# Performance work log

Measured on AMD Instinct MI355X. Metric: run time of the kernel, lower is better.

## Reference

```python
import jax, jax.numpy as jnp
import numpy as np

PERIODS = [4, 2, 1]   # base_periods[:n_period]
TEMPERATURE = 0.1
TOPM = 20
EPS = 1e-12


def _l2norm(v, axis):
    n = jnp.sqrt(jnp.sum(v * v, axis=axis, keepdims=True))
    return v / jnp.maximum(n, EPS)


def decompose_mg(x):
    """x: [B, L, C] -> mg: [G, B, L, C] (offset removed, as in torch code)."""
    B, L, C = x.shape
    mg = []
    for g in PERIODS:
        cur = x.reshape(B, L // g, g, C).mean(axis=2)      # unfold(size=g, step=g).mean(-1)
        cur = jnp.repeat(cur, g, axis=1)                   # repeat_interleave back to L
        mg.append(cur)
    mg = jnp.stack(mg, axis=0)                             # [G, B, L, C]
    return mg - mg[:, :, -1:, :]                           # remove per-series last-step offset


def extract_channel_state(mg):
    """mg: [G, B, L, C] -> [G, B, C, 4] (mean, std, slope, mean |diff|)."""
    L = mg.shape[2]
    mean = mg.mean(axis=2)
    std = mg.std(axis=2)                                   # unbiased=False (ddof=0)
    slope = (mg[:, :, -1, :] - mg[:, :, 0, :]) / float(L - 1)
    abs_diff = jnp.abs(mg[:, :, 1:, :] - mg[:, :, :-1, :]).mean(axis=2)
    return jnp.stack([mean, std, slope, abs_diff], axis=-1)


def setup_inputs() -> dict:
    key = jax.random.key(0)
    k1, k2, k3 = jax.random.split(key, 3)
    B, L, C, G, T, P = 32, 512, 64, 3, 10000, 96
    x = jax.random.normal(k1, (B, L, C), dtype=jnp.float32)
    pool_state = jax.random.normal(k2, (G, T, C, 4), dtype=jnp.float32)
    y_pool = jax.random.normal(k3, (T, P, C), dtype=jnp.float32)
    return {"x": x, "pool_state": pool_state, "y_pool": y_pool}


def reference(x, pool_state, y_pool):
    # Multi-scale decomposition of query batch
    q_mg = decompose_mg(x)                                  # [G, B, L, C]
    q_state = extract_channel_state(q_mg)                   # [G, B, C, 4]
    # Normalized channel-state similarity vs candidate pool
    q = _l2norm(q_state, axis=-1)
    p = _l2norm(pool_state, axis=-1)
    sim = jnp.einsum('gbcd,gtcd->gbct', q, p)               # [G, B, C, T]
    sim = sim.mean(axis=0)                                  # combine granularities -> [B, C, T]
    # Top-m retrieval per (batch, channel)
    vals, idx = jax.lax.top_k(sim, TOPM)                    # [B, C, M]
    w = jax.nn.softmax(vals / TEMPERATURE, axis=-1)         # [B, C, M]
    # Gather retrieved future windows, channelwise: y_pool [T, P, C]
    C = y_pool.shape[2]
    y_ct = jnp.transpose(y_pool, (2, 0, 1))                 # [C, T, P]
    gathered = y_ct[jnp.arange(C)[None, :, None], idx]      # [B, C, M, P]
    out = jnp.einsum('bcm,bcmp->bpc', w, gathered)          # [B, P, C]
    return out
```

## Files before the change

kernel.cpp:

```cpp
#include <hip/hip_runtime.h>
#include <math.h>

#define NB 32
#define NL 512
#define NC 64
#define NG 3
#define NT 10000
#define NP 96
#define TOPM 20
#define M1 8
#define NCH 256
#define CHUNK 40
#define QK 16
#define NCAND 64
#define GSTR ((size_t)NT * NC * 4)

__global__ __launch_bounds__(512) void pre_kernel(const float* __restrict__ x,
                                                  const float* __restrict__ ps,
                                                  double* __restrict__ q,
                                                  float* __restrict__ phat) {
  __shared__ double s_sum[8][3][64], s_sq[8][3][64], s_abs[8][3][64];
  __shared__ double s_first[3][64], s_last[3][64];
  if (blockIdx.x < NB) {
    const int b = blockIdx.x, w = threadIdx.x >> 6, c = threadIdx.x & 63;
    const float* xp = x + (size_t)b * NL * NC + c;
    const int l0 = w * 64;
    double sum[3] = {0, 0, 0}, sumsq[3] = {0, 0, 0}, sumabs[3] = {0, 0, 0};
    double prev[3] = {0, 0, 0}, first[3] = {0, 0, 0};
    if (w > 0) {
      double e0 = xp[(l0 - 4) * NC], e1 = xp[(l0 - 3) * NC];
      double e2 = xp[(l0 - 2) * NC], e3 = xp[(l0 - 1) * NC];
      prev[2] = e3; prev[1] = (e2 + e3) * 0.5; prev[0] = (e0 + e1 + e2 + e3) * 0.25;
    }
    double acc2 = 0.0, acc4 = 0.0;
    for (int i = 0; i < 64; ++i) {
      const int l = l0 + i;
      double v = (double)xp[l * NC];
      sum[2] += v; sumsq[2] += v * v;
      if (l == 0) first[2] = v; else sumabs[2] += fabs(v - prev[2]);
      prev[2] = v;
      acc2 += v;
      if (l & 1) {
        double cur = acc2 * 0.5; acc2 = 0.0;
        sum[1] += cur; sumsq[1] += cur * cur;
        if (l == 1) first[1] = cur; else sumabs[1] += fabs(cur - prev[1]);
        prev[1] = cur;
      }
      acc4 += v;
      if ((l & 3) == 3) {
        double cur = acc4 * 0.25; acc4 = 0.0;
        sum[0] += cur; sumsq[0] += cur * cur;
        if (l == 3) first[0] = cur; else sumabs[0] += fabs(cur - prev[0]);
        prev[0] = cur;
      }
    }
    for (int g = 0; g < 3; ++g) {
      s_sum[w][g][c] = sum[g]; s_sq[w][g][c] = sumsq[g]; s_abs[w][g][c] = sumabs[g];
    }
    if (w == 0) { for (int g = 0; g < 3; ++g) s_first[g][c] = first[g]; }
    if (w == 7) { for (int g = 0; g < 3; ++g) s_last[g][c] = prev[g]; }
    __syncthreads();
    if (w == 0) {
      const double J[3] = {128.0, 256.0, 512.0};
      for (int g = 0; g < 3; ++g) {
        double S = 0, Q2 = 0, A = 0;
        for (int ww = 0; ww < 8; ++ww) {
          S += s_sum[ww][g][c]; Q2 += s_sq[ww][g][c]; A += s_abs[ww][g][c];
        }
        double mean = S / J[g];
        double var = Q2 / J[g] - mean * mean; if (var < 0.0) var = 0.0;
        double last = s_last[g][c];
        double s0 = mean - last;
        double s1 = sqrt(var);
        double s2 = (last - s_first[g][c]) * (1.0 / 511.0);
        double s3 = A * (1.0 / 511.0);
        double n = sqrt(s0 * s0 + s1 * s1 + s2 * s2 + s3 * s3);
        double inv = 1.0 / fmax(n, 1e-12);
        double* qp = q + ((((size_t)g * NB) + b) * NC + c) * 4;
        qp[0] = s0 * inv; qp[1] = s1 * inv; qp[2] = s2 * inv; qp[3] = s3 * inv;
      }
    }
  } else {
    const int i = (blockIdx.x - NB) * 512 + threadIdx.x;
    if (i < NT * NC) {
      const int t = i >> 6, c = i & 63;
#pragma unroll
      for (int g = 0; g < 3; ++g) {
        const size_t off = ((((size_t)g * NT) + t) * NC + c) * 4;
        const float4 pv = *reinterpret_cast<const float4*>(ps + off);
        double p0 = pv.x, p1 = pv.y, p2 = pv.z, p3 = pv.w;
        double inv = 1.0 / fmax(sqrt(p0 * p0 + p1 * p1 + p2 * p2 + p3 * p3), 1e-12);
        float4 o;
        o.x = (float)(p0 * inv); o.y = (float)(p1 * inv);
        o.z = (float)(p2 * inv); o.w = (float)(p3 * inv);
        *reinterpret_cast<float4*>(phat + off) = o;
      }
    }
  }
}

__device__ __forceinline__ void insert8(float s, int ti, float val[M1], int idx[M1]) {
  float cv = s; int ci = ti;
#pragma unroll
  for (int m = 0; m < M1; ++m) {
    bool sw = cv > val[m];
    float tv = sw ? val[m] : cv; int tx = sw ? idx[m] : ci;
    val[m] = sw ? cv : val[m];   idx[m] = sw ? ci : idx[m];
    cv = tv; ci = tx;
  }
}

__global__ __launch_bounds__(1024, 8) void sim32_kernel(
    const float* __restrict__ phat, const double* __restrict__ q,
    float* __restrict__ cval, int* __restrict__ cidx) {
  const int wav = threadIdx.x >> 6;
  const int c = threadIdx.x & 63;
  const int b = blockIdx.x * 16 + wav;
  const int ch = blockIdx.y;
  float qv[12];
#pragma unroll
  for (int g = 0; g < 3; ++g) {
    const double* qp = q + ((((size_t)g * NB) + b) * NC + c) * 4;
#pragma unroll
    for (int j = 0; j < 4; ++j) qv[g * 4 + j] = (float)(qp[j] * (1.0 / 3.0));
  }
  float val[M1]; int idx[M1];
#pragma unroll
  for (int m = 0; m < M1; ++m) { val[m] = -1e30f; idx[m] = 0; }
  int t0 = ch * CHUNK;
  int t1 = t0 + CHUNK; if (t1 > NT) t1 = NT;
  for (int t = t0; t + 1 < t1; t += 2) {
    const size_t oA = ((size_t)t * NC + c) * 4;
    const size_t oB = ((size_t)(t + 1) * NC + c) * 4;
    const float4 a0 = *reinterpret_cast<const float4*>(phat + oA);
    const float4 a1 = *reinterpret_cast<const float4*>(phat + GSTR + oA);
    const float4 a2 = *reinterpret_cast<const float4*>(phat + 2 * GSTR + oA);
    const float4 b0 = *reinterpret_cast<const float4*>(phat + oB);
    const float4 b1 = *reinterpret_cast<const float4*>(phat + GSTR + oB);
    const float4 b2 = *reinterpret_cast<const float4*>(phat + 2 * GSTR + oB);
    float sA = qv[0] * a0.x + qv[1] * a0.y + qv[2] * a0.z + qv[3] * a0.w +
               qv[4] * a1.x + qv[5] * a1.y + qv[6] * a1.z + qv[7] * a1.w +
               qv[8] * a2.x + qv[9] * a2.y + qv[10] * a2.z + qv[11] * a2.w;
    float sB = qv[0] * b0.x + qv[1] * b0.y + qv[2] * b0.z + qv[3] * b0.w +
               qv[4] * b1.x + qv[5] * b1.y + qv[6] * b1.z + qv[7] * b1.w +
               qv[8] * b2.x + qv[9] * b2.y + qv[10] * b2.z + qv[11] * b2.w;
    if (sA > val[M1 - 1]) insert8(sA, t, val, idx);
    if (sB > val[M1 - 1]) insert8(sB, t + 1, val, idx);
  }
  float* vo = cval + ((((size_t)b * NC) + c) * NCH + ch) * M1;
  int* io = cidx + ((((size_t)b * NC) + c) * NCH + ch) * M1;
#pragma unroll
  for (int m = 0; m < M1; ++m) { vo[m] = val[m]; io[m] = idx[m]; }
}

__device__ __forceinline__ unsigned long long mk_key(float v, int t) {
  unsigned u = __float_as_uint(v);
  u = (u & 0x80000000u) ? ~u : (u | 0x80000000u);
  return ((unsigned long long)u << 32) | (unsigned long long)(0xFFFFFFFFu - (unsigned)t);
}

__global__ __launch_bounds__(128) void merge_gather_kernel(
    const float* __restrict__ cval, const int* __restrict__ cidx,
    const float* __restrict__ ps, const double* __restrict__ q,
    const float* __restrict__ y, float* __restrict__ out) {
  const int c = blockIdx.x, b = blockIdx.y;
  __shared__ float v_s[NCH * M1];
  __shared__ int i_s[NCH * M1];
  __shared__ int ct_s[NCAND];
  __shared__ double rv_s[NCAND];
  __shared__ double m0_s, inv_s;
  __shared__ double e_s[TOPM];
  __shared__ float w_s[TOPM];
  __shared__ int ts_s[TOPM];
  const int n = NCH * M1;
  const size_t row = (size_t)b * NC + c;
  const float4* vin = reinterpret_cast<const float4*>(cval + row * n);
  const int4* iin = reinterpret_cast<const int4*>(cidx + row * n);
  for (int k = threadIdx.x; k < n / 4; k += 128) {
    *reinterpret_cast<float4*>(&v_s[k * 4]) = vin[k];
    *reinterpret_cast<int4*>(&i_s[k * 4]) = iin[k];
  }
  __syncthreads();
  {
    const int w = threadIdx.x >> 6, lane = threadIdx.x & 63;
    const int lane32 = lane & 31;
    const int qtr = (w << 1) | (lane >> 5);
    const int l0 = (qtr * 64 + lane32 * 2) * M1;
    const int l1 = l0 + M1;
    int p0 = 0, p1 = 0;
    unsigned long long k0 = mk_key(v_s[l0], i_s[l0]);
    unsigned long long k1 = mk_key(v_s[l1], i_s[l1]);
    for (int r = 0; r < QK; ++r) {
      unsigned long long me = k0 > k1 ? k0 : k1;
      unsigned long long km = me;
#pragma unroll
      for (int st = 1; st < 32; st <<= 1) {
        unsigned long long k2 = __shfl_xor(km, st);
        km = k2 > km ? k2 : km;
      }
      if (lane32 == r)
        ct_s[qtr * QK + r] = (int)(0xFFFFFFFFu - (unsigned)(km & 0xFFFFFFFFull));
      if (me == km) {
        if (k0 >= k1) {
          ++p0;
          k0 = (p0 < M1) ? mk_key(v_s[l0 + p0], i_s[l0 + p0]) : 0ull;
        } else {
          ++p1;
          k1 = (p1 < M1) ? mk_key(v_s[l1 + p1], i_s[l1 + p1]) : 0ull;
        }
      }
    }
  }
  __syncthreads();
  if (threadIdx.x < NCAND) {
    const int t = ct_s[threadIdx.x];
    double s = 0.0;
#pragma unroll
    for (int g = 0; g < 3; ++g) {
      const double* qp = q + ((((size_t)g * NB) + b) * NC + c) * 4;
      const float4 pv = *reinterpret_cast<const float4*>(
          ps + ((((size_t)g * NT) + t) * NC + c) * 4);
      double pp0 = pv.x, pp1 = pv.y, pp2 = pv.z, pp3 = pv.w;
      double ss = pp0 * pp0 + pp1 * pp1 + pp2 * pp2 + pp3 * pp3;
      double dot = qp[0] * pp0 + qp[1] * pp1 + qp[2] * pp2 + qp[3] * pp3;
      s += dot / fmax(sqrt(ss), 1e-12);
    }
    rv_s[threadIdx.x] = s * (1.0 / 3.0);
  }
  __syncthreads();
  if (threadIdx.x < NCAND) {
    const double v = rv_s[threadIdx.x];
    const int t = ct_s[threadIdx.x];
    int rank = 0;
    for (int j = 0; j < NCAND; ++j) {
      double vj = rv_s[j]; int tj = ct_s[j];
      rank += (vj > v) || (vj == v && tj < t);
    }
    if (rank == 0) m0_s = v;
    __syncthreads();
    if (rank < TOPM) {
      e_s[rank] = exp((v - m0_s) * 10.0);
      ts_s[rank] = t;
    }
    __syncthreads();
    if (threadIdx.x == 0) {
      double sum = 0.0;
#pragma unroll
      for (int m = 0; m < TOPM; ++m) sum += e_s[m];
      inv_s = 1.0 / sum;
    }
    __syncthreads();
    if (threadIdx.x < TOPM) w_s[threadIdx.x] = (float)(e_s[threadIdx.x] * inv_s);
  } else {
    __syncthreads(); __syncthreads(); __syncthreads();
  }
  __syncthreads();
  const int p = threadIdx.x;
  if (p < NP) {
    float acc = 0.f;
#pragma unroll
    for (int m = 0; m < TOPM; ++m)
      acc += w_s[m] * y[(((size_t)ts_s[m]) * NP + p) * NC + c];
    out[(((size_t)b * NP) + p) * NC + c] = acc;
  }
}

__global__ __launch_bounds__(256) void sim_topk_inline_kernel(
    const float* __restrict__ ps, const double* __restrict__ q,
    double* __restrict__ cval, int* __restrict__ cidx, int nch, int chunk) {
  const int wav = threadIdx.x >> 6;
  const int c = threadIdx.x & 63;
  const int b = blockIdx.y * 4 + wav;
  const int ch = blockIdx.x;
  double qv[3][4];
#pragma unroll
  for (int g = 0; g < 3; ++g) {
    const double* qp = q + ((((size_t)g * NB) + b) * NC + c) * 4;
    qv[g][0] = qp[0]; qv[g][1] = qp[1]; qv[g][2] = qp[2]; qv[g][3] = qp[3];
  }
  double val[TOPM]; int idx[TOPM];
#pragma unroll
  for (int m = 0; m < TOPM; ++m) { val[m] = -1e300; idx[m] = 0; }
  int t0 = ch * chunk;
  int t1 = t0 + chunk; if (t1 > NT) t1 = NT;
  for (int t = t0; t < t1; ++t) {
    double s = 0.0;
#pragma unroll
    for (int g = 0; g < 3; ++g) {
      const float4 pv = *reinterpret_cast<const float4*>(
          ps + ((((size_t)g * NT) + t) * NC + c) * 4);
      double p0 = pv.x, p1 = pv.y, p2 = pv.z, p3 = pv.w;
      double ss = p0 * p0 + p1 * p1 + p2 * p2 + p3 * p3;
      double dot = qv[g][0] * p0 + qv[g][1] * p1 + qv[g][2] * p2 + qv[g][3] * p3;
      s += dot / fmax(sqrt(ss), 1e-12);
    }
    s *= (1.0 / 3.0);
    if (s > val[TOPM - 1]) {
// ... 40 lines not shown
          cv = tv; ci = ti;
        }
      }
    }
    double mx = val[0];
    double e[TOPM]; double sum = 0.0;
#pragma unroll
    for (int m = 0; m < TOPM; ++m) { e[m] = exp((val[m] - mx) * 10.0); sum += e[m]; }
    double inv = 1.0 / sum;
#pragma unroll
    for (int m = 0; m < TOPM; ++m) { w_s[m] = (float)(e[m] * inv); i_s[m] = idx[m]; }
  }
  __syncthreads();
  const int p = threadIdx.x;
  if (p < NP) {
    float acc = 0.f;
#pragma unroll
    for (int m = 0; m < TOPM; ++m)
      acc += w_s[m] * y[(((size_t)i_s[m]) * NP + p) * NC + c];
    out[(((size_t)b * NP) + p) * NC + c] = acc;
  }
}

extern "C" void kernel_launch(void* const* d_in, const int* in_sizes, int n_in,
                              void* d_out, int out_size, void* d_ws, size_t ws_size,
                              hipStream_t stream) {
  const float* x = (const float*)d_in[0];
  const float* ps = (const float*)d_in[1];
  const float* y = (const float*)d_in[2];
  float* out = (float*)d_out;
  char* ws = (char*)d_ws;

  const size_t qbytes = (size_t)NG * NB * NC * 4 * sizeof(double);
  const size_t phat32bytes = (size_t)NG * NT * NC * 4 * sizeof(float);
  const size_t cvalbytes = (size_t)NB * NC * NCH * M1 * sizeof(float);
  const size_t cidxbytes = (size_t)NB * NC * NCH * M1 * sizeof(int);

  double* qbuf = (double*)ws;

  if (ws_size >= qbytes + phat32bytes + cvalbytes + cidxbytes) {
    float* phat = (float*)(ws + qbytes);
    float* cval = (float*)(ws + qbytes + phat32bytes);
    int* cidx = (int*)((char*)cval + cvalbytes);
    const int pn_blocks = (NT * NC + 511) / 512;
    pre_kernel<<<dim3(NB + pn_blocks), dim3(512), 0, stream>>>(x, ps, qbuf, phat);
    sim32_kernel<<<dim3(NB / 16, NCH), dim3(1024), 0, stream>>>(phat, qbuf, cval, cidx);
    merge_gather_kernel<<<dim3(NC, NB), dim3(128), 0, stream>>>(cval, cidx, ps, qbuf,
                                                                y, out);
  } else {
    pre_kernel<<<dim3(NB), dim3(512), 0, stream>>>(x, ps, qbuf, (float*)nullptr);
    const size_t per_ch = (size_t)NB * NC * TOPM * (sizeof(double) + sizeof(int));
    int nch = 1;
    if (ws_size > qbytes) {
      size_t mc = (ws_size - qbytes) / per_ch;
      nch = mc < 32 ? (int)mc : 32;
      if (nch < 1) nch = 1;
    }
    const int chunk = (NT + nch - 1) / nch;
    double* cval = (double*)(ws + qbytes);
    int* cidx = (int*)((char*)cval + (size_t)NB * NC * nch * TOPM * sizeof(double));
    sim_topk_inline_kernel<<<dim3(nch, NB / 4), dim3(256), 0, stream>>>(
        ps, qbuf, cval, cidx, nch, chunk);
    merge_gather_old_kernel<<<dim3(NC, NB), dim3(128), 0, stream>>>(cval, cidx, y, out, nch);
  }
}
```

Measured before the change: 139.1 us.

## Fuse pool normalization into similarity kernel and pack candidates into one buffer

Removes the separate pass that normalized pool_state into a float workspace copy. The similarity kernel now reads raw pool_state and applies rsqrt-based normalization inline, which avoids writing and re-reading a ~30MB buffer but adds per-element normalization math. Candidate values and indices are packed into one interleaved 64-byte record per chunk and written with vector stores. The merge/gather kernel grows to 256 threads and splits the 20-way gather across two halves, with indices sorted for locality. Launch bounds on the sim kernel drop from occupancy 8 to 4.

```diff
diff --git a/kernel.cpp b/kernel.cpp
--- a/kernel.cpp
+++ b/kernel.cpp
@@ -15,86 +15,66 @@
 #define NCAND 64
 #define GSTR ((size_t)NT * NC * 4)
 
-__global__ __launch_bounds__(512) void pre_kernel(const float* __restrict__ x,
-                                                  const float* __restrict__ ps,
-                                                  double* __restrict__ q,
-                                                  float* __restrict__ phat) {
+__global__ __launch_bounds__(512) void qstat_kernel(const float* __restrict__ x,
+                                                    double* __restrict__ q) {
   __shared__ double s_sum[8][3][64], s_sq[8][3][64], s_abs[8][3][64];
   __shared__ double s_first[3][64], s_last[3][64];
-  if (blockIdx.x < NB) {
-    const int b = blockIdx.x, w = threadIdx.x >> 6, c = threadIdx.x & 63;
-    const float* xp = x + (size_t)b * NL * NC + c;
-    const int l0 = w * 64;
-    double sum[3] = {0, 0, 0}, sumsq[3] = {0, 0, 0}, sumabs[3] = {0, 0, 0};
-    double prev[3] = {0, 0, 0}, first[3] = {0, 0, 0};
-    if (w > 0) {
-      double e0 = xp[(l0 - 4) * NC], e1 = xp[(l0 - 3) * NC];
-      double e2 = xp[(l0 - 2) * NC], e3 = xp[(l0 - 1) * NC];
-      prev[2] = e3; prev[1] = (e2 + e3) * 0.5; prev[0] = (e0 + e1 + e2 + e3) * 0.25;
-    }
-    double acc2 = 0.0, acc4 = 0.0;
-    for (int i = 0; i < 64; ++i) {
-      const int l = l0 + i;
-      double v = (double)xp[l * NC];
-      sum[2] += v; sumsq[2] += v * v;
-      if (l == 0) first[2] = v; else sumabs[2] += fabs(v - prev[2]);
-      prev[2] = v;
-      acc2 += v;
-      if (l & 1) {
-        double cur = acc2 * 0.5; acc2 = 0.0;
-        sum[1] += cur; sumsq[1] += cur * cur;
-        if (l == 1) first[1] = cur; else sumabs[1] += fabs(cur - prev[1]);
-        prev[1] = cur;
+  const int b = blockIdx.x, w = threadIdx.x >> 6, c = threadIdx.x & 63;
+  const float* xp = x + (size_t)b * NL * NC + c;
+  const int l0 = w * 64;
+  double sum[3] = {0, 0, 0}, sumsq[3] = {0, 0, 0}, sumabs[3] = {0, 0, 0};
+  double prev[3] = {0, 0, 0}, first[3] = {0, 0, 0};
+  if (w > 0) {
+    double e0 = xp[(l0 - 4) * NC], e1 = xp[(l0 - 3) * NC];
+    double e2 = xp[(l0 - 2) * NC], e3 = xp[(l0 - 1) * NC];
+    prev[2] = e3; prev[1] = (e2 + e3) * 0.5; prev[0] = (e0 + e1 + e2 + e3) * 0.25;
+  }
+  double acc2 = 0.0, acc4 = 0.0;
+  for (int i = 0; i < 64; ++i) {
+    const int l = l0 + i;
+    double v = (double)xp[l * NC];
+    sum[2] += v; sumsq[2] += v * v;
+    if (l == 0) first[2] = v; else sumabs[2] += fabs(v - prev[2]);
+    prev[2] = v;
+    acc2 += v;
+    if (l & 1) {
+      double cur = acc2 * 0.5; acc2 = 0.0;
+      sum[1] += cur; sumsq[1] += cur * cur;
+      if (l == 1) first[1] = cur; else sumabs[1] += fabs(cur - prev[1]);
+      prev[1] = cur;
+    }
+    acc4 += v;
+    if ((l & 3) == 3) {
+      double cur = acc4 * 0.25; acc4 = 0.0;
+      sum[0] += cur; sumsq[0] += cur * cur;
+      if (l == 3) first[0] = cur; else sumabs[0] += fabs(cur - prev[0]);
+      prev[0] = cur;
+    }
+  }
+  for (int g = 0; g < 3; ++g) {
+    s_sum[w][g][c] = sum[g]; s_sq[w][g][c] = sumsq[g]; s_abs[w][g][c] = sumabs[g];
+  }
+  if (w == 0) { for (int g = 0; g < 3; ++g) s_first[g][c] = first[g]; }
+  if (w == 7) { for (int g = 0; g < 3; ++g) s_last[g][c] = prev[g]; }
+  __syncthreads();
+  if (w == 0) {
+    const double J[3] = {128.0, 256.0, 512.0};
+    for (int g = 0; g < 3; ++g) {
+      double S = 0, Q2 = 0, A = 0;
+      for (int ww = 0; ww < 8; ++ww) {
+        S += s_sum[ww][g][c]; Q2 += s_sq[ww][g][c]; A += s_abs[ww][g][c];
       }
-      acc4 += v;
-      if ((l & 3) == 3) {
-        double cur = acc4 * 0.25; acc4 = 0.0;
-        sum[0] += cur; sumsq[0] += cur * cur;
-        if (l == 3) first[0] = cur; else sumabs[0] += fabs(cur - prev[0]);
-        prev[0] = cur;
-      }
-    }
-    for (int g = 0; g < 3; ++g) {
-      s_sum[w][g][c] = sum[g]; s_sq[w][g][c] = sumsq[g]; s_abs[w][g][c] = sumabs[g];
-    }
-    if (w == 0) { for (int g = 0; g < 3; ++g) s_first[g][c] = first[g]; }
-    if (w == 7) { for (int g = 0; g < 3; ++g) s_last[g][c] = prev[g]; }
-    __syncthreads();
-    if (w == 0) {
-      const double J[3] = {128.0, 256.0, 512.0};
-      for (int g = 0; g < 3; ++g) {
-        double S = 0, Q2 = 0, A = 0;
-        for (int ww = 0; ww < 8; ++ww) {
-          S += s_sum[ww][g][c]; Q2 += s_sq[ww][g][c]; A += s_abs[ww][g][c];
-        }
-        double mean = S / J[g];
-        double var = Q2 / J[g] - mean * mean; if (var < 0.0) var = 0.0;
-        double last = s_last[g][c];
-        double s0 = mean - last;
-        double s1 = sqrt(var);
-        double s2 = (last - s_first[g][c]) * (1.0 / 511.0);
-        double s3 = A * (1.0 / 511.0);
-        double n = sqrt(s0 * s0 + s1 * s1 + s2 * s2 + s3 * s3);
-        double inv = 1.0 / fmax(n, 1e-12);
-        double* qp = q + ((((size_t)g * NB) + b) * NC + c) * 4;
-        qp[0] = s0 * inv; qp[1] = s1 * inv; qp[2] = s2 * inv; qp[3] = s3 * inv;
-      }
-    }
-  } else {
-    const int i = (blockIdx.x - NB) * 512 + threadIdx.x;
-    if (i < NT * NC) {
-      const int t = i >> 6, c = i & 63;
-#pragma unroll
-      for (int g = 0; g < 3; ++g) {
-        const size_t off = ((((size_t)g * NT) + t) * NC + c) * 4;
-        const float4 pv = *reinterpret_cast<const float4*>(ps + off);
-        double p0 = pv.x, p1 = pv.y, p2 = pv.z, p3 = pv.w;
-        double inv = 1.0 / fmax(sqrt(p0 * p0 + p1 * p1 + p2 * p2 + p3 * p3), 1e-12);
-        float4 o;
-        o.x = (float)(p0 * inv); o.y = (float)(p1 * inv);
-        o.z = (float)(p2 * inv); o.w = (float)(p3 * inv);
-        *reinterpret_cast<float4*>(phat + off) = o;
-      }
+      double mean = S / J[g];
+      double var = Q2 / J[g] - mean * mean; if (var < 0.0) var = 0.0;
+      double last = s_last[g][c];
+      double s0 = mean - last;
+      double s1 = sqrt(var);
+      double s2 = (last - s_first[g][c]) * (1.0 / 511.0);
+      double s3 = A * (1.0 / 511.0);
+      double n = sqrt(s0 * s0 + s1 * s1 + s2 * s2 + s3 * s3);
+      double inv = 1.0 / fmax(n, 1e-12);
+      double* qp = q + ((((size_t)g * NB) + b) * NC + c) * 4;
+      qp[0] = s0 * inv; qp[1] = s1 * inv; qp[2] = s2 * inv; qp[3] = s3 * inv;
     }
   }
 }
@@ -110,9 +90,17 @@
   }
 }
 
-__global__ __launch_bounds__(1024, 8) void sim32_kernel(
-    const float* __restrict__ phat, const double* __restrict__ q,
-    float* __restrict__ cval, int* __restrict__ cidx) {
+__device__ __forceinline__ float dot4(float4 a, float q0, float q1, float q2, float q3) {
+  return q0 * a.x + q1 * a.y + q2 * a.z + q3 * a.w;
+}
+__device__ __forceinline__ float nrm4(float4 a) {
+  float ss = a.x * a.x + a.y * a.y + a.z * a.z + a.w * a.w;
+  return rsqrtf(ss < 1e-24f ? 1e-24f : ss);
+}
+
+__global__ __launch_bounds__(1024, 4) void sim32_kernel(
+    const float* __restrict__ ps, const double* __restrict__ q,
+    float* __restrict__ cand) {
   const int wav = threadIdx.x >> 6;
   const int c = threadIdx.x & 63;
   const int b = blockIdx.x * 16 + wav;
@@ -131,26 +119,31 @@
   int t1 = t0 + CHUNK; if (t1 > NT) t1 = NT;
   for (int t = t0; t + 1 < t1; t += 2) {
     const size_t oA = ((size_t)t * NC + c) * 4;
-    const size_t oB = ((size_t)(t + 1) * NC + c) * 4;
-    const float4 a0 = *reinterpret_cast<const float4*>(phat + oA);
-    const float4 a1 = *reinterpret_cast<const float4*>(phat + GSTR + oA);
-    const float4 a2 = *reinterpret_cast<const float4*>(phat + 2 * GSTR + oA);
-    const float4 b0 = *reinterpret_cast<const float4*>(phat + oB);
-    const float4 b1 = *reinterpret_cast<const float4*>(phat + GSTR + oB);
-    const float4 b2 = *reinterpret_cast<const float4*>(phat + 2 * GSTR + oB);
-    float sA = qv[0] * a0.x + qv[1] * a0.y + qv[2] * a0.z + qv[3] * a0.w +
-               qv[4] * a1.x + qv[5] * a1.y + qv[6] * a1.z + qv[7] * a1.w +
-               qv[8] * a2.x + qv[9] * a2.y + qv[10] * a2.z + qv[11] * a2.w;
-    float sB = qv[0] * b0.x + qv[1] * b0.y + qv[2] * b0.z + qv[3] * b0.w +
-               qv[4] * b1.x + qv[5] * b1.y + qv[6] * b1.z + qv[7] * b1.w +
-               qv[8] * b2.x + qv[9] * b2.y + qv[10] * b2.z + qv[11] * b2.w;
+    const size_t oB = oA + (size_t)NC * 4;
+    const float4 a0 = *reinterpret_cast<const float4*>(ps + oA);
+    const float4 a1 = *reinterpret_cast<const float4*>(ps + GSTR + oA);
+    const float4 a2 = *reinterpret_cast<const float4*>(ps + 2 * GSTR + oA);
+    const float4 b0 = *reinterpret_cast<const float4*>(ps + oB);
+    const float4 b1 = *reinterpret_cast<const float4*>(ps + GSTR + oB);
+    const float4 b2 = *reinterpret_cast<const float4*>(ps + 2 * GSTR + oB);
+    float sA = dot4(a0, qv[0], qv[1], qv[2], qv[3]) * nrm4(a0) +
+               dot4(a1, qv[4], qv[5], qv[6], qv[7]) * nrm4(a1) +
+               dot4(a2, qv[8], qv[9], qv[10], qv[11]) * nrm4(a2);
+    float sB = dot4(b0, qv[0], qv[1], qv[2], qv[3]) * nrm4(b0) +
+               dot4(b1, qv[4], qv[5], qv[6], qv[7]) * nrm4(b1) +
+               dot4(b2, qv[8], qv[9], qv[10], qv[11]) * nrm4(b2);
     if (sA > val[M1 - 1]) insert8(sA, t, val, idx);
     if (sB > val[M1 - 1]) insert8(sB, t + 1, val, idx);
   }
-  float* vo = cval + ((((size_t)b * NC) + c) * NCH + ch) * M1;
-  int* io = cidx + ((((size_t)b * NC) + c) * NCH + ch) * M1;
-#pragma unroll
-  for (int m = 0; m < M1; ++m) { vo[m] = val[m]; io[m] = idx[m]; }
+  float* bp = cand + ((((size_t)b * NC) + c) * NCH + ch) * 16;
+  float4 f0 = make_float4(val[0], val[1], val[2], val[3]);
+  float4 f1 = make_float4(val[4], val[5], val[6], val[7]);
+  int4 j0 = make_int4(idx[0], idx[1], idx[2], idx[3]);
+  int4 j1 = make_int4(idx[4], idx[5], idx[6], idx[7]);
+  reinterpret_cast<float4*>(bp)[0] = f0;
+  reinterpret_cast<float4*>(bp)[1] = f1;
+  reinterpret_cast<int4*>(bp)[2] = j0;
+  reinterpret_cast<int4*>(bp)[3] = j1;
 }
 
 __device__ __forceinline__ unsigned long long mk_key(float v, int t) {
@@ -159,10 +152,10 @@
   return ((unsigned long long)u << 32) | (unsigned long long)(0xFFFFFFFFu - (unsigned)t);
 }
 
-__global__ __launch_bounds__(128) void merge_gather_kernel(
-    const float* __restrict__ cval, const int* __restrict__ cidx,
-    const float* __restrict__ ps, const double* __restrict__ q,
-    const float* __restrict__ y, float* __restrict__ out) {
+__global__ __launch_bounds__(256) void merge_gather_kernel(
+    const float* __restrict__ cand, const float* __restrict__ ps,
+    const double* __restrict__ q, const float* __restrict__ y,
+    float* __restrict__ out) {
   const int c = blockIdx.x, b = blockIdx.y;
   __shared__ float v_s[NCH * M1];
   __shared__ int i_s[NCH * M1];
@@ -170,18 +163,26 @@
   __shared__ double rv_s[NCAND];
   __shared__ double m0_s, inv_s;
   __shared__ double e_s[TOPM];
-  __shared__ float w_s[TOPM];
   __shared__ int ts_s[TOPM];
-  const int n = NCH * M1;
+  __shared__ float w2_s[TOPM];
+  __shared__ int t2_s[TOPM];
+  __shared__ float part_s[2][NP];
   const size_t row = (size_t)b * NC + c;
-  const float4* vin = reinterpret_cast<const float4*>(cval + row * n);
-  const int4* iin = reinterpret_cast<const int4*>(cidx + row * n);
-  for (int k = threadIdx.x; k < n / 4; k += 128) {
-    *reinterpret_cast<float4*>(&v_s[k * 4]) = vin[k];
-    *reinterpret_cast<int4*>(&i_s[k * 4]) = iin[k];
-  }
-  __syncthreads();
-  {
+  const float4* blob = reinterpret_cast<const float4*>(cand + row * NCH * 16);
+  for (int k = threadIdx.x; k < NCH * 4; k += 256) {
+    float4 f = blob[k];
+    const int ch = k >> 2, part = k & 3;
+    if (part < 2) {
+      const int o = ch * M1 + part * 4;
+      v_s[o] = f.x; v_s[o + 1] = f.y; v_s[o + 2] = f.z; v_s[o + 3] = f.w;
+    } else {
+      const int o = ch * M1 + (part - 2) * 4;
+      int4 j = *reinterpret_cast<int4*>(&f);
+      i_s[o] = j.x; i_s[o + 1] = j.y; i_s[o + 2] = j.z; i_s[o + 3] = j.w;
+    }
+  }
+  __syncthreads();
+  if (threadIdx.x < 128) {
     const int w = threadIdx.x >> 6, lane = threadIdx.x & 63;
     const int lane32 = lane & 31;
     const int qtr = (w << 1) | (lane >> 5);
@@ -202,67 +203,76 @@
         ct_s[qtr * QK + r] = (int)(0xFFFFFFFFu - (unsigned)(km & 0xFFFFFFFFull));
       if (me == km) {
         if (k0 >= k1) {
-          ++p0;
-          k0 = (p0 < M1) ? mk_key(v_s[l0 + p0], i_s[l0 + p0]) : 0ull;
+          ++p0; k0 = (p0 < M1) ? mk_key(v_s[l0 + p0], i_s[l0 + p0]) : 0ull;
         } else {
-          ++p1;
-          k1 = (p1 < M1) ? mk_key(v_s[l1 + p1], i_s[l1 + p1]) : 0ull;
+          ++p1; k1 = (p1 < M1) ? mk_key(v_s[l1 + p1], i_s[l1 + p1]) : 0ull;
         }
       }
     }
   }
   __syncthreads();
+  double myv = -1e300; int myt = 0x7fffffff;
   if (threadIdx.x < NCAND) {
-    const int t = ct_s[threadIdx.x];
+    myt = ct_s[threadIdx.x];
     double s = 0.0;
 #pragma unroll
     for (int g = 0; g < 3; ++g) {
       const double* qp = q + ((((size_t)g * NB) + b) * NC + c) * 4;
       const float4 pv = *reinterpret_cast<const float4*>(
-          ps + ((((size_t)g * NT) + t) * NC + c) * 4);
+          ps + ((((size_t)g * NT) + myt) * NC + c) * 4);
       double pp0 = pv.x, pp1 = pv.y, pp2 = pv.z, pp3 = pv.w;
       double ss = pp0 * pp0 + pp1 * pp1 + pp2 * pp2 + pp3 * pp3;
       double dot = qp[0] * pp0 + qp[1] * pp1 + qp[2] * pp2 + qp[3] * pp3;
       s += dot / fmax(sqrt(ss), 1e-12);
     }
-    rv_s[threadIdx.x] = s * (1.0 / 3.0);
-  }
-  __syncthreads();
+    myv = s * (1.0 / 3.0);
+    rv_s[threadIdx.x] = myv;
+  }
+  __syncthreads();
+  int rank = -1;
   if (threadIdx.x < NCAND) {
-    const double v = rv_s[threadIdx.x];
-    const int t = ct_s[threadIdx.x];
-    int rank = 0;
+    rank = 0;
     for (int j = 0; j < NCAND; ++j) {
       double vj = rv_s[j]; int tj = ct_s[j];
-      rank += (vj > v) || (vj == v && tj < t);
-    }
-    if (rank == 0) m0_s = v;
-    __syncthreads();
-    if (rank < TOPM) {
-      e_s[rank] = exp((v - m0_s) * 10.0);
-      ts_s[rank] = t;
-    }
-    __syncthreads();
-    if (threadIdx.x == 0) {
-      double sum = 0.0;
-#pragma unroll
-      for (int m = 0; m < TOPM; ++m) sum += e_s[m];
-      inv_s = 1.0 / sum;
-    }
-    __syncthreads();
-    if (threadIdx.x < TOPM) w_s[threadIdx.x] = (float)(e_s[threadIdx.x] * inv_s);
-  } else {
-    __syncthreads(); __syncthreads(); __syncthreads();
-  }
-  __syncthreads();
-  const int p = threadIdx.x;
-  if (p < NP) {
+      rank += (vj > myv) || (vj == myv && tj < myt);
+    }
+    if (rank == 0) m0_s = myv;
+  }
+  __syncthreads();
+  if (rank >= 0 && rank < TOPM) { e_s[rank] = exp((myv - m0_s) * 10.0); ts_s[rank] = myt; }
+  __syncthreads();
+  if (threadIdx.x == 0) {
+    double sum = 0.0;
+#pragma unroll
+    for (int m = 0; m < TOPM; ++m) sum += e_s[m];
+    inv_s = 1.0 / sum;
+  }
+  __syncthreads();
+  if (threadIdx.x < TOPM) {
+    const int t = ts_s[threadIdx.x];
+    int pos = 0;
+#pragma unroll
+    for (int j = 0; j < TOPM; ++j) pos += (ts_s[j] < t);
+    w2_s[pos] = (float)(e_s[threadIdx.x] * inv_s);
+    t2_s[pos] = t;
+  }
+  __syncthreads();
+  const int half = threadIdx.x >> 7;
+  const int pp = threadIdx.x & 127;
+  if (pp < NP) {
     float acc = 0.f;
-#pragma unroll
-    for (int m = 0; m < TOPM; ++m)
-      acc += w_s[m] * y[(((size_t)ts_s[m]) * NP + p) * NC + c];
-    out[(((size_t)b * NP) + p) * NC + c] = acc;
-  }
+    const float* yc = y + c;
+#pragma unroll
+    for (int m = 0; m < 10; ++m) {
+      const int mm = half * 10 + m;
+      acc += w2_s[mm] * yc[((size_t)t2_s[mm] * NP + pp) << 6];
+    }
+    part_s[half][pp] = acc;
+  }
+  __syncthreads();
+  if (threadIdx.x < NP)
+    out[(((size_t)b * NP) + threadIdx.x) * NC + c] =
+        part_s[0][threadIdx.x] + part_s[1][threadIdx.x];
 }
 
 __global__ __launch_bounds__(256) void sim_topk_inline_kernel(
@@ -369,23 +379,17 @@
   char* ws = (char*)d_ws;
 
   const size_t qbytes = (size_t)NG * NB * NC * 4 * sizeof(double);
-  const size_t phat32bytes = (size_t)NG * NT * NC * 4 * sizeof(float);
-  const size_t cvalbytes = (size_t)NB * NC * NCH * M1 * sizeof(float);
-  const size_t cidxbytes = (size_t)NB * NC * NCH * M1 * sizeof(int);
+  const size_t candbytes = (size_t)NB * NC * NCH * 16 * sizeof(float);
 
   double* qbuf = (double*)ws;
 
-  if (ws_size >= qbytes + phat32bytes + cvalbytes + cidxbytes) {
-    float* phat = (float*)(ws + qbytes);
-    float* cval = (float*)(ws + qbytes + phat32bytes);
-    int* cidx = (int*)((char*)cval + cvalbytes);
-    const int pn_blocks = (NT * NC + 511) / 512;
-    pre_kernel<<<dim3(NB + pn_blocks), dim3(512), 0, stream>>>(x, ps, qbuf, phat);
-    sim32_kernel<<<dim3(NB / 16, NCH), dim3(1024), 0, stream>>>(phat, qbuf, cval, cidx);
-    merge_gather_kernel<<<dim3(NC, NB), dim3(128), 0, stream>>>(cval, cidx, ps, qbuf,
-                                                                y, out);
+  if (ws_size >= qbytes + candbytes) {
+    float* cand = (float*)(ws + qbytes);
+    qstat_kernel<<<dim3(NB), dim3(512), 0, stream>>>(x, qbuf);
+    sim32_kernel<<<dim3(NB / 16, NCH), dim3(1024), 0, stream>>>(ps, qbuf, cand);
+    merge_gather_kernel<<<dim3(NC, NB), dim3(256), 0, stream>>>(cand, ps, qbuf, y, out);
   } else {
-    pre_kernel<<<dim3(NB), dim3(512), 0, stream>>>(x, ps, qbuf, (float*)nullptr);
+    qstat_kernel<<<dim3(NB), dim3(512), 0, stream>>>(x, qbuf);
     const size_t per_ch = (size_t)NB * NC * TOPM * (sizeof(double) + sizeof(int));
     int nch = 1;
     if (ws_size > qbytes) {
```

Result: slower. 156.2 us (+12.3%).

## Pre-transpose y_pool to channel-major fp16 for contiguous gather reads

Applied to the files above, without the earlier changes.

Adds a block range to the prep kernel that transposes the 236 MB y_pool into a [C,T,P] half-precision buffer via LDS, so the final gather reads contiguous P-runs per channel instead of strided 4-byte loads. The transpose runs every call and must read all of y_pool and write a 123 MB buffer, which is far more traffic than the sparse gather (B*C*20*96 elements) it replaces. Output precision also drops to fp16 for the retrieved windows. The merge kernel's synchronization structure is also flattened.

```diff
diff --git a/kernel.cpp b/kernel.cpp
--- a/kernel.cpp
+++ b/kernel.cpp
@@ -1,4 +1,5 @@
 #include <hip/hip_runtime.h>
+#include <hip/hip_fp16.h>
 #include <math.h>
 
 #define NB 32
@@ -13,15 +14,21 @@
 #define CHUNK 40
 #define QK 16
 #define NCAND 64
+#define PNBLK 1250
+#define TRBLK 5000
 #define GSTR ((size_t)NT * NC * 4)
 
-__global__ __launch_bounds__(512) void pre_kernel(const float* __restrict__ x,
-                                                  const float* __restrict__ ps,
-                                                  double* __restrict__ q,
-                                                  float* __restrict__ phat) {
-  __shared__ double s_sum[8][3][64], s_sq[8][3][64], s_abs[8][3][64];
-  __shared__ double s_first[3][64], s_last[3][64];
+__global__ __launch_bounds__(512) void prep_kernel(
+    const float* __restrict__ x, const float* __restrict__ ps,
+    const float* __restrict__ y, double* __restrict__ q,
+    float* __restrict__ phat, __half* __restrict__ yt16) {
+  __shared__ __align__(16) char smem[50176];
   if (blockIdx.x < NB) {
+    double* s_sum = (double*)smem;
+    double* s_sq = s_sum + 1536;
+    double* s_abs = s_sq + 1536;
+    double* s_first = s_abs + 1536;
+    double* s_last = s_first + 192;
     const int b = blockIdx.x, w = threadIdx.x >> 6, c = threadIdx.x & 63;
     const float* xp = x + (size_t)b * NL * NC + c;
     const int l0 = w * 64;
@@ -55,24 +62,28 @@
       }
     }
     for (int g = 0; g < 3; ++g) {
-      s_sum[w][g][c] = sum[g]; s_sq[w][g][c] = sumsq[g]; s_abs[w][g][c] = sumabs[g];
-    }
-    if (w == 0) { for (int g = 0; g < 3; ++g) s_first[g][c] = first[g]; }
-    if (w == 7) { for (int g = 0; g < 3; ++g) s_last[g][c] = prev[g]; }
+      s_sum[w * 192 + g * 64 + c] = sum[g];
+      s_sq[w * 192 + g * 64 + c] = sumsq[g];
+      s_abs[w * 192 + g * 64 + c] = sumabs[g];
+    }
+    if (w == 0) { for (int g = 0; g < 3; ++g) s_first[g * 64 + c] = first[g]; }
+    if (w == 7) { for (int g = 0; g < 3; ++g) s_last[g * 64 + c] = prev[g]; }
     __syncthreads();
     if (w == 0) {
       const double J[3] = {128.0, 256.0, 512.0};
       for (int g = 0; g < 3; ++g) {
         double S = 0, Q2 = 0, A = 0;
         for (int ww = 0; ww < 8; ++ww) {
-          S += s_sum[ww][g][c]; Q2 += s_sq[ww][g][c]; A += s_abs[ww][g][c];
+          S += s_sum[ww * 192 + g * 64 + c];
+          Q2 += s_sq[ww * 192 + g * 64 + c];
+          A += s_abs[ww * 192 + g * 64 + c];
         }
         double mean = S / J[g];
         double var = Q2 / J[g] - mean * mean; if (var < 0.0) var = 0.0;
-        double last = s_last[g][c];
+        double last = s_last[g * 64 + c];
         double s0 = mean - last;
         double s1 = sqrt(var);
-        double s2 = (last - s_first[g][c]) * (1.0 / 511.0);
+        double s2 = (last - s_first[g * 64 + c]) * (1.0 / 511.0);
         double s3 = A * (1.0 / 511.0);
         double n = sqrt(s0 * s0 + s1 * s1 + s2 * s2 + s3 * s3);
         double inv = 1.0 / fmax(n, 1e-12);
@@ -80,7 +91,7 @@
         qp[0] = s0 * inv; qp[1] = s1 * inv; qp[2] = s2 * inv; qp[3] = s3 * inv;
       }
     }
-  } else {
+  } else if (blockIdx.x < NB + PNBLK) {
     const int i = (blockIdx.x - NB) * 512 + threadIdx.x;
     if (i < NT * NC) {
       const int t = i >> 6, c = i & 63;
@@ -96,6 +107,30 @@
         *reinterpret_cast<float4*>(phat + off) = o;
       }
     }
+  } else {
+    float* lds = (float*)smem;
+    const int tb = blockIdx.x - NB - PNBLK;
+    const int T0 = (tb % 1250) * 8;
+    const int C0 = (tb / 1250) * 16;
+    for (int i = threadIdx.x; i < 3072; i += 512) {
+      const int cq = i & 3, p = (i >> 2) % 96, t = i / 384;
+      const float4 v = *reinterpret_cast<const float4*>(
+          y + ((size_t)(T0 + t) * NP + p) * NC + C0 + cq * 4);
+      const int cb = cq * 4;
+      lds[(cb + 0) * 784 + t * 98 + p] = v.x;
+      lds[(cb + 1) * 784 + t * 98 + p] = v.y;
+      lds[(cb + 2) * 784 + t * 98 + p] = v.z;
+      lds[(cb + 3) * 784 + t * 98 + p] = v.w;
+    }
+    __syncthreads();
+    for (int j = threadIdx.x; j < 6144; j += 512) {
+      const int p2 = j % 48, t = (j / 48) & 7, c = j / 384;
+      const float a = lds[c * 784 + t * 98 + p2 * 2];
+      const float bb = lds[c * 784 + t * 98 + p2 * 2 + 1];
+      const __half2 h = __halves2half2(__float2half_rn(a), __float2half_rn(bb));
+      *reinterpret_cast<__half2*>(
+          yt16 + ((size_t)(C0 + c) * NT + T0 + t) * NP + p2 * 2) = h;
+    }
   }
 }
 
@@ -131,7 +166,7 @@
   int t1 = t0 + CHUNK; if (t1 > NT) t1 = NT;
   for (int t = t0; t + 1 < t1; t += 2) {
     const size_t oA = ((size_t)t * NC + c) * 4;
-    const size_t oB = ((size_t)(t + 1) * NC + c) * 4;
+    const size_t oB = oA + (size_t)NC * 4;
     const float4 a0 = *reinterpret_cast<const float4*>(phat + oA);
     const float4 a1 = *reinterpret_cast<const float4*>(phat + GSTR + oA);
     const float4 a2 = *reinterpret_cast<const float4*>(phat + 2 * GSTR + oA);
@@ -162,7 +197,7 @@
 __global__ __launch_bounds__(128) void merge_gather_kernel(
     const float* __restrict__ cval, const int* __restrict__ cidx,
     const float* __restrict__ ps, const double* __restrict__ q,
-    const float* __restrict__ y, float* __restrict__ out) {
+    const __half* __restrict__ yt16, float* __restrict__ out) {
   const int c = blockIdx.x, b = blockIdx.y;
   __shared__ float v_s[NCH * M1];
   __shared__ int i_s[NCH * M1];
@@ -170,8 +205,8 @@
   __shared__ double rv_s[NCAND];
   __shared__ double m0_s, inv_s;
   __shared__ double e_s[TOPM];
+  __shared__ int ts_s[TOPM];
   __shared__ float w_s[TOPM];
-  __shared__ int ts_s[TOPM];
   const int n = NCH * M1;
   const size_t row = (size_t)b * NC + c;
   const float4* vin = reinterpret_cast<const float4*>(cval + row * n);
@@ -202,65 +237,60 @@
         ct_s[qtr * QK + r] = (int)(0xFFFFFFFFu - (unsigned)(km & 0xFFFFFFFFull));
       if (me == km) {
         if (k0 >= k1) {
-          ++p0;
-          k0 = (p0 < M1) ? mk_key(v_s[l0 + p0], i_s[l0 + p0]) : 0ull;
+          ++p0; k0 = (p0 < M1) ? mk_key(v_s[l0 + p0], i_s[l0 + p0]) : 0ull;
         } else {
-          ++p1;
-          k1 = (p1 < M1) ? mk_key(v_s[l1 + p1], i_s[l1 + p1]) : 0ull;
+          ++p1; k1 = (p1 < M1) ? mk_key(v_s[l1 + p1], i_s[l1 + p1]) : 0ull;
         }
       }
     }
   }
   __syncthreads();
+  double myv = -1e300; int myt = 0x7fffffff;
   if (threadIdx.x < NCAND) {
-    const int t = ct_s[threadIdx.x];
+    myt = ct_s[threadIdx.x];
     double s = 0.0;
 #pragma unroll
     for (int g = 0; g < 3; ++g) {
       const double* qp = q + ((((size_t)g * NB) + b) * NC + c) * 4;
       const float4 pv = *reinterpret_cast<const float4*>(
-          ps + ((((size_t)g * NT) + t) * NC + c) * 4);
+          ps + ((((size_t)g * NT) + myt) * NC + c) * 4);
       double pp0 = pv.x, pp1 = pv.y, pp2 = pv.z, pp3 = pv.w;
       double ss = pp0 * pp0 + pp1 * pp1 + pp2 * pp2 + pp3 * pp3;
       double dot = qp[0] * pp0 + qp[1] * pp1 + qp[2] * pp2 + qp[3] * pp3;
       s += dot / fmax(sqrt(ss), 1e-12);
     }
-    rv_s[threadIdx.x] = s * (1.0 / 3.0);
-  }
-  __syncthreads();
+    myv = s * (1.0 / 3.0);
+    rv_s[threadIdx.x] = myv;
+  }
+  __syncthreads();
+  int rank = -1;
   if (threadIdx.x < NCAND) {
-    const double v = rv_s[threadIdx.x];
-    const int t = ct_s[threadIdx.x];
-    int rank = 0;
+    rank = 0;
     for (int j = 0; j < NCAND; ++j) {
       double vj = rv_s[j]; int tj = ct_s[j];
-      rank += (vj > v) || (vj == v && tj < t);
-    }
-    if (rank == 0) m0_s = v;
-    __syncthreads();
-    if (rank < TOPM) {
-      e_s[rank] = exp((v - m0_s) * 10.0);
-      ts_s[rank] = t;
-    }
-    __syncthreads();
-    if (threadIdx.x == 0) {
-      double sum = 0.0;
-#pragma unroll
-      for (int m = 0; m < TOPM; ++m) sum += e_s[m];
-      inv_s = 1.0 / sum;
-    }
-    __syncthreads();
-    if (threadIdx.x < TOPM) w_s[threadIdx.x] = (float)(e_s[threadIdx.x] * inv_s);
-  } else {
-    __syncthreads(); __syncthreads(); __syncthreads();
-  }
+      rank += (vj > myv) || (vj == myv && tj < myt);
+    }
+    if (rank == 0) m0_s = myv;
+  }
+  __syncthreads();
+  if (rank >= 0 && rank < TOPM) { e_s[rank] = exp((myv - m0_s) * 10.0); ts_s[rank] = myt; }
+  __syncthreads();
+  if (threadIdx.x == 0) {
+    double sum = 0.0;
+#pragma unroll
+    for (int m = 0; m < TOPM; ++m) sum += e_s[m];
+    inv_s = 1.0 / sum;
+  }
+  __syncthreads();
+  if (threadIdx.x < TOPM) w_s[threadIdx.x] = (float)(e_s[threadIdx.x] * inv_s);
   __syncthreads();
   const int p = threadIdx.x;
   if (p < NP) {
+    const __half* yc = yt16 + (size_t)c * NT * NP + p;
     float acc = 0.f;
 #pragma unroll
     for (int m = 0; m < TOPM; ++m)
-      acc += w_s[m] * y[(((size_t)ts_s[m]) * NP + p) * NC + c];
+      acc += w_s[m] * __half2float(yc[(size_t)ts_s[m] * NP]);
     out[(((size_t)b * NP) + p) * NC + c] = acc;
   }
 }
@@ -369,23 +399,26 @@
   char* ws = (char*)d_ws;
 
   const size_t qbytes = (size_t)NG * NB * NC * 4 * sizeof(double);
-  const size_t phat32bytes = (size_t)NG * NT * NC * 4 * sizeof(float);
+  const size_t phatbytes = (size_t)NG * NT * NC * 4 * sizeof(float);
   const size_t cvalbytes = (size_t)NB * NC * NCH * M1 * sizeof(float);
   const size_t cidxbytes = (size_t)NB * NC * NCH * M1 * sizeof(int);
+  const size_t ytbytes = (size_t)NC * NT * NP * sizeof(__half);
 
   double* qbuf = (double*)ws;
 
-  if (ws_size >= qbytes + phat32bytes + cvalbytes + cidxbytes) {
+  if (ws_size >= qbytes + phatbytes + cvalbytes + cidxbytes + ytbytes) {
     float* phat = (float*)(ws + qbytes);
-    float* cval = (float*)(ws + qbytes + phat32bytes);
+    float* cval = (float*)(ws + qbytes + phatbytes);
     int* cidx = (int*)((char*)cval + cvalbytes);
-    const int pn_blocks = (NT * NC + 511) / 512;
-    pre_kernel<<<dim3(NB + pn_blocks), dim3(512), 0, stream>>>(x, ps, qbuf, phat);
+    __half* yt16 = (__half*)((char*)cidx + cidxbytes);
+    prep_kernel<<<dim3(NB + PNBLK + TRBLK), dim3(512), 0, stream>>>(
+        x, ps, y, qbuf, phat, yt16);
     sim32_kernel<<<dim3(NB / 16, NCH), dim3(1024), 0, stream>>>(phat, qbuf, cval, cidx);
     merge_gather_kernel<<<dim3(NC, NB), dim3(128), 0, stream>>>(cval, cidx, ps, qbuf,
-                                                                y, out);
+                                                                yt16, out);
   } else {
-    pre_kernel<<<dim3(NB), dim3(512), 0, stream>>>(x, ps, qbuf, (float*)nullptr);
+    prep_kernel<<<dim3(NB), dim3(512), 0, stream>>>(x, ps, y, qbuf,
+                                                    (float*)nullptr, (__half*)nullptr);
     const size_t per_ch = (size_t)NB * NC * TOPM * (sizeof(double) + sizeof(int));
     int nch = 1;
     if (ws_size > qbytes) {
```

New measurement: 218.4 us. +57.0%, slower.

## Bin retrieved indices by pool row to read each y row once

Applied to the files above, without the earlier changes.

The gather stage is restructured. The old code had each (b,c) block read 20 scattered y columns with stride NC. The new code builds a histogram of the selected t indices, runs a prefix scan and scatter to group entries by t, and has one block per pool row load that row of y into LDS before writing weighted partials. A final kernel then sums the 20 partials per (b,c). The aim is coalesced, single-pass reads of y. The cost is four extra launches, atomics, a single-block scan, a 10000-block process grid and a large partial buffer written and read back.

```diff
diff --git a/kernel.cpp b/kernel.cpp
--- a/kernel.cpp
+++ b/kernel.cpp
@@ -13,6 +13,8 @@
 #define CHUNK 40
 #define QK 16
 #define NCAND 64
+#define PNBLK 1250
+#define NENT (NB * NC * TOPM)
 #define GSTR ((size_t)NT * NC * 4)
 
 __global__ __launch_bounds__(512) void pre_kernel(const float* __restrict__ x,
@@ -112,7 +114,11 @@
 
 __global__ __launch_bounds__(1024, 8) void sim32_kernel(
     const float* __restrict__ phat, const double* __restrict__ q,
-    float* __restrict__ cval, int* __restrict__ cidx) {
+    float* __restrict__ cval, int* __restrict__ cidx, int* __restrict__ hist) {
+  if (blockIdx.x == 0 && blockIdx.y < 10) {
+    const int idx = blockIdx.y * 1024 + threadIdx.x;
+    if (idx < NT) hist[idx] = 0;
+  }
   const int wav = threadIdx.x >> 6;
   const int c = threadIdx.x & 63;
   const int b = blockIdx.x * 16 + wav;
@@ -131,7 +137,7 @@
   int t1 = t0 + CHUNK; if (t1 > NT) t1 = NT;
   for (int t = t0; t + 1 < t1; t += 2) {
     const size_t oA = ((size_t)t * NC + c) * 4;
-    const size_t oB = ((size_t)(t + 1) * NC + c) * 4;
+    const size_t oB = oA + (size_t)NC * 4;
     const float4 a0 = *reinterpret_cast<const float4*>(phat + oA);
     const float4 a1 = *reinterpret_cast<const float4*>(phat + GSTR + oA);
     const float4 a2 = *reinterpret_cast<const float4*>(phat + 2 * GSTR + oA);
@@ -159,10 +165,10 @@
   return ((unsigned long long)u << 32) | (unsigned long long)(0xFFFFFFFFu - (unsigned)t);
 }
 
-__global__ __launch_bounds__(128) void merge_gather_kernel(
+__global__ __launch_bounds__(128) void merge_rerank_kernel(
     const float* __restrict__ cval, const int* __restrict__ cidx,
     const float* __restrict__ ps, const double* __restrict__ q,
-    const float* __restrict__ y, float* __restrict__ out) {
+    float* __restrict__ w_out, int* __restrict__ t_out, int* __restrict__ hist) {
   const int c = blockIdx.x, b = blockIdx.y;
   __shared__ float v_s[NCH * M1];
   __shared__ int i_s[NCH * M1];
@@ -170,7 +176,6 @@
   __shared__ double rv_s[NCAND];
   __shared__ double m0_s, inv_s;
   __shared__ double e_s[TOPM];
-  __shared__ float w_s[TOPM];
   __shared__ int ts_s[TOPM];
   const int n = NCH * M1;
   const size_t row = (size_t)b * NC + c;
@@ -202,67 +207,145 @@
         ct_s[qtr * QK + r] = (int)(0xFFFFFFFFu - (unsigned)(km & 0xFFFFFFFFull));
       if (me == km) {
         if (k0 >= k1) {
-          ++p0;
-          k0 = (p0 < M1) ? mk_key(v_s[l0 + p0], i_s[l0 + p0]) : 0ull;
+          ++p0; k0 = (p0 < M1) ? mk_key(v_s[l0 + p0], i_s[l0 + p0]) : 0ull;
         } else {
-          ++p1;
-          k1 = (p1 < M1) ? mk_key(v_s[l1 + p1], i_s[l1 + p1]) : 0ull;
+          ++p1; k1 = (p1 < M1) ? mk_key(v_s[l1 + p1], i_s[l1 + p1]) : 0ull;
         }
       }
     }
   }
   __syncthreads();
+  double myv = -1e300; int myt = 0x7fffffff;
   if (threadIdx.x < NCAND) {
-    const int t = ct_s[threadIdx.x];
+    myt = ct_s[threadIdx.x];
     double s = 0.0;
 #pragma unroll
     for (int g = 0; g < 3; ++g) {
       const double* qp = q + ((((size_t)g * NB) + b) * NC + c) * 4;
       const float4 pv = *reinterpret_cast<const float4*>(
-          ps + ((((size_t)g * NT) + t) * NC + c) * 4);
+          ps + ((((size_t)g * NT) + myt) * NC + c) * 4);
       double pp0 = pv.x, pp1 = pv.y, pp2 = pv.z, pp3 = pv.w;
       double ss = pp0 * pp0 + pp1 * pp1 + pp2 * pp2 + pp3 * pp3;
       double dot = qp[0] * pp0 + qp[1] * pp1 + qp[2] * pp2 + qp[3] * pp3;
       s += dot / fmax(sqrt(ss), 1e-12);
     }
-    rv_s[threadIdx.x] = s * (1.0 / 3.0);
-  }
-  __syncthreads();
+    myv = s * (1.0 / 3.0);
+    rv_s[threadIdx.x] = myv;
+  }
+  __syncthreads();
+  int rank = -1;
   if (threadIdx.x < NCAND) {
-    const double v = rv_s[threadIdx.x];
-    const int t = ct_s[threadIdx.x];
-    int rank = 0;
+    rank = 0;
     for (int j = 0; j < NCAND; ++j) {
       double vj = rv_s[j]; int tj = ct_s[j];
-      rank += (vj > v) || (vj == v && tj < t);
-    }
-    if (rank == 0) m0_s = v;
+      rank += (vj > myv) || (vj == myv && tj < myt);
+    }
+    if (rank == 0) m0_s = myv;
+  }
+  __syncthreads();
+  if (rank >= 0 && rank < TOPM) { e_s[rank] = exp((myv - m0_s) * 10.0); ts_s[rank] = myt; }
+  __syncthreads();
+  if (threadIdx.x == 0) {
+    double sum = 0.0;
+#pragma unroll
+    for (int m = 0; m < TOPM; ++m) sum += e_s[m];
+    inv_s = 1.0 / sum;
+  }
+  __syncthreads();
+  if (threadIdx.x < TOPM) {
+    const int t = ts_s[threadIdx.x];
+    w_out[row * TOPM + threadIdx.x] = (float)(e_s[threadIdx.x] * inv_s);
+    t_out[row * TOPM + threadIdx.x] = t;
+    atomicAdd(&hist[t], 1);
+  }
+}
+
+__global__ __launch_bounds__(1024) void scan_kernel(const int* __restrict__ hist,
+                                                    int* __restrict__ bin_off,
+                                                    int* __restrict__ cursor) {
+  __shared__ int part[1024];
+  const int tid = threadIdx.x;
+  int loc[10];
+  int s = 0;
+#pragma unroll
+  for (int j = 0; j < 10; ++j) {
+    const int idx = tid * 10 + j;
+    const int v = (idx < NT) ? hist[idx] : 0;
+    loc[j] = s;
+    s += v;
+  }
+  part[tid] = s;
+  __syncthreads();
+  for (int st = 1; st < 1024; st <<= 1) {
+    const int v = (tid >= st) ? part[tid - st] : 0;
     __syncthreads();
-    if (rank < TOPM) {
-      e_s[rank] = exp((v - m0_s) * 10.0);
-      ts_s[rank] = t;
-    }
+    part[tid] += v;
     __syncthreads();
-    if (threadIdx.x == 0) {
-      double sum = 0.0;
-#pragma unroll
-      for (int m = 0; m < TOPM; ++m) sum += e_s[m];
-      inv_s = 1.0 / sum;
-    }
-    __syncthreads();
-    if (threadIdx.x < TOPM) w_s[threadIdx.x] = (float)(e_s[threadIdx.x] * inv_s);
-  } else {
-    __syncthreads(); __syncthreads(); __syncthreads();
+  }
+  const int base = (tid == 0) ? 0 : part[tid - 1];
+#pragma unroll
+  for (int j = 0; j < 10; ++j) {
+    const int idx = tid * 10 + j;
+    if (idx < NT) {
+      const int off = base + loc[j];
+      bin_off[idx] = off;
+      cursor[idx] = off;
+    }
+  }
+  if (tid == 1023) bin_off[NT] = part[1023];
+}
+
+__global__ __launch_bounds__(256) void scatter_kernel(
+    const int* __restrict__ t_out, int* __restrict__ cursor,
+    int* __restrict__ bin_slot) {
+  const int i = blockIdx.x * 256 + threadIdx.x;
+  if (i < NENT) {
+    const int t = t_out[i];
+    const int pos = atomicAdd(&cursor[t], 1);
+    bin_slot[pos] = i;
+  }
+}
+
+__global__ __launch_bounds__(128) void process_kernel(
+    const float* __restrict__ y, const int* __restrict__ bin_off,
+    const int* __restrict__ bin_slot, const float* __restrict__ w_out,
+    float* __restrict__ partial) {
+  const int t = blockIdx.x;
+  const int start = bin_off[t];
+  const int k = bin_off[t + 1] - start;
+  if (k == 0) return;
+  __shared__ float lds[NP * 65];
+  const float4* yrow = reinterpret_cast<const float4*>(y + (size_t)t * NP * NC);
+#pragma unroll
+  for (int r = 0; r < 12; ++r) {
+    const int e4 = threadIdx.x + r * 128;
+    const float4 v = yrow[e4];
+    const int p = e4 >> 4;
+    const int c = (e4 & 15) * 4;
+    lds[p * 65 + c] = v.x; lds[p * 65 + c + 1] = v.y;
+    lds[p * 65 + c + 2] = v.z; lds[p * 65 + c + 3] = v.w;
   }
   __syncthreads();
   const int p = threadIdx.x;
-  if (p < NP) {
-    float acc = 0.f;
-#pragma unroll
-    for (int m = 0; m < TOPM; ++m)
-      acc += w_s[m] * y[(((size_t)ts_s[m]) * NP + p) * NC + c];
-    out[(((size_t)b * NP) + p) * NC + c] = acc;
-  }
+  for (int e = 0; e < k; ++e) {
+    const int i = bin_slot[start + e];
+    const float w = w_out[i];
+    const int c = (i / TOPM) & 63;
+    if (p < NP) partial[(size_t)i * NP + p] = w * lds[p * 65 + c];
+  }
+}
+
+__global__ __launch_bounds__(128) void final_kernel(const float* __restrict__ partial,
+                                                    float* __restrict__ out) {
+  const int row = blockIdx.x;
+  const int p = threadIdx.x;
+  if (p >= NP) return;
+  const int b = row >> 6, c = row & 63;
+  const float* pp = partial + (size_t)row * TOPM * NP + p;
+  float acc = 0.f;
+#pragma unroll
+  for (int m = 0; m < TOPM; ++m) acc += pp[m * NP];
+  out[(((size_t)b * NP) + p) * NC + c] = acc;
 }
 
 __global__ __launch_bounds__(256) void sim_topk_inline_kernel(
@@ -369,21 +452,40 @@
   char* ws = (char*)d_ws;
 
   const size_t qbytes = (size_t)NG * NB * NC * 4 * sizeof(double);
-  const size_t phat32bytes = (size_t)NG * NT * NC * 4 * sizeof(float);
+  const size_t phatbytes = (size_t)NG * NT * NC * 4 * sizeof(float);
   const size_t cvalbytes = (size_t)NB * NC * NCH * M1 * sizeof(float);
-  const size_t cidxbytes = (size_t)NB * NC * NCH * M1 * sizeof(int);
+  const size_t cidxbytes = cvalbytes;
+  const size_t wtbytes = (size_t)NENT * sizeof(float);
+  const size_t histbytes = (size_t)NT * sizeof(int);
+  const size_t offbytes = (size_t)(NT + 4) * sizeof(int);
+  const size_t slotbytes = (size_t)NENT * sizeof(int);
+  const size_t partbytes = (size_t)NENT * NP * sizeof(float);
 
   double* qbuf = (double*)ws;
-
-  if (ws_size >= qbytes + phat32bytes + cvalbytes + cidxbytes) {
-    float* phat = (float*)(ws + qbytes);
-    float* cval = (float*)(ws + qbytes + phat32bytes);
-    int* cidx = (int*)((char*)cval + cvalbytes);
-    const int pn_blocks = (NT * NC + 511) / 512;
-    pre_kernel<<<dim3(NB + pn_blocks), dim3(512), 0, stream>>>(x, ps, qbuf, phat);
-    sim32_kernel<<<dim3(NB / 16, NCH), dim3(1024), 0, stream>>>(phat, qbuf, cval, cidx);
-    merge_gather_kernel<<<dim3(NC, NB), dim3(128), 0, stream>>>(cval, cidx, ps, qbuf,
-                                                                y, out);
+  size_t off = qbytes;
+  float* phat = (float*)(ws + off); off += phatbytes;
+  float* cval = (float*)(ws + off); off += cvalbytes;
+  int* cidx = (int*)(ws + off); off += cidxbytes;
+  float* w_out = (float*)(ws + off); off += wtbytes;
+  int* t_out = (int*)(ws + off); off += wtbytes;
+  int* hist = (int*)(ws + off); off += histbytes;
+  int* bin_off = (int*)(ws + off); off += offbytes;
+  int* cursor = (int*)(ws + off); off += histbytes;
+  int* bin_slot = (int*)(ws + off); off += slotbytes;
+  float* partial = (float*)(ws + off); off += partbytes;
+
+  if (ws_size >= off) {
+    pre_kernel<<<dim3(NB + PNBLK), dim3(512), 0, stream>>>(x, ps, qbuf, phat);
+    sim32_kernel<<<dim3(NB / 16, NCH), dim3(1024), 0, stream>>>(phat, qbuf, cval,
+                                                                cidx, hist);
+    merge_rerank_kernel<<<dim3(NC, NB), dim3(128), 0, stream>>>(
+        cval, cidx, ps, qbuf, w_out, t_out, hist);
+    scan_kernel<<<dim3(1), dim3(1024), 0, stream>>>(hist, bin_off, cursor);
+    scatter_kernel<<<dim3((NENT + 255) / 256), dim3(256), 0, stream>>>(
+        t_out, cursor, bin_slot);
+    process_kernel<<<dim3(NT), dim3(128), 0, stream>>>(y, bin_off, bin_slot,
+                                                       w_out, partial);
+    final_kernel<<<dim3(NB * NC), dim3(128), 0, stream>>>(partial, out);
   } else {
     pre_kernel<<<dim3(NB), dim3(512), 0, stream>>>(x, ps, qbuf, (float*)nullptr);
     const size_t per_ch = (size_t)NB * NC * TOPM * (sizeof(double) + sizeof(int));
@@ -394,10 +496,11 @@
       if (nch < 1) nch = 1;
     }
     const int chunk = (NT + nch - 1) / nch;
-    double* cval = (double*)(ws + qbytes);
-    int* cidx = (int*)((char*)cval + (size_t)NB * NC * nch * TOPM * sizeof(double));
+    double* fcval = (double*)(ws + qbytes);
+    int* fcidx = (int*)((char*)fcval + (size_t)NB * NC * nch * TOPM * sizeof(double));
     sim_topk_inline_kernel<<<dim3(nch, NB / 4), dim3(256), 0, stream>>>(
-        ps, qbuf, cval, cidx, nch, chunk);
-    merge_gather_old_kernel<<<dim3(NC, NB), dim3(128), 0, stream>>>(cval, cidx, y, out, nch);
-  }
-}
+        ps, qbuf, fcval, fcidx, nch, chunk);
+    merge_gather_old_kernel<<<dim3(NC, NB), dim3(128), 0, stream>>>(fcval, fcidx, y,
+                                                                    out, nch);
+  }
+}
```

After: 153.0 us. +9.9%, slower.
